# Kernel tuning notes

Hardware: AMD Instinct MI355X
Metric: run time of the kernel (lower is better)

## Reference

```python
import jax, jax.numpy as jnp
import numpy as np


def setup_inputs() -> dict:
    key = jax.random.key(0)
    ks = jax.random.split(key, 9)
    B, S, F = 16, 512, 1024
    scale = 1.0 / np.sqrt(2 * F)  # ~torch Linear init scale
    return {
        "v": jax.random.normal(ks[0], (B, S, F), jnp.float32),
        "t": jax.random.normal(ks[1], (B, S, F), jnp.float32),
        "a": jax.random.normal(ks[2], (B, S, F), jnp.float32),
        "W_tv": jax.random.normal(ks[3], (2 * F, F), jnp.float32) * scale,
        "b_tv": jnp.zeros((F,), jnp.float32),
        "W_ta": jax.random.normal(ks[4], (2 * F, F), jnp.float32) * scale,
        "b_ta": jnp.zeros((F,), jnp.float32),
        "W_av": jax.random.normal(ks[5], (2 * F, F), jnp.float32) * scale,
        "b_av": jnp.zeros((F,), jnp.float32),
    }


def _branch_feat(x1, x2, W, b):
    # tanh(Linear(cat(x1, x2)))  -- split weight to avoid materializing concat
    F = x1.shape[-1]
    W1, W2 = W[:F], W[F:]
    return jnp.tanh(jnp.einsum("bsf,fg->bsg", x1, W1)
                    + jnp.einsum("bsf,fg->bsg", x2, W2) + b)


def _attend_gate(q, feat):
    # softmax(q @ feat^T) @ q, gated by feat
    scores = jnp.einsum("bqf,bkf->bqk", q, feat)  # [B,S,S]
    p = jax.nn.softmax(scores, axis=-1)
    return jnp.einsum("bqk,bkf->bqf", p, q) * feat


def reference(v, t, a, W_tv, b_tv, W_ta, b_ta, W_av, b_av):
    Ftv = _branch_feat(t, v, W_tv, b_tv)
    Fta = _branch_feat(t, a, W_ta, b_ta)
    Fav = _branch_feat(a, v, W_av, b_av)
    Oatv = _attend_gate(a, Ftv)
    Ovta = _attend_gate(v, Fta)
    Otav = _attend_gate(t, Fav)
    return jnp.concatenate((Oatv, Ovta, Otav), axis=2)
```

## Files before the change

kernel.cpp:

```cpp
#include <hip/hip_runtime.h>

typedef unsigned short ushort_t;
typedef _Float16 f16x8 __attribute__((ext_vector_type(8)));
typedef float f32x4 __attribute__((ext_vector_type(4)));
typedef unsigned short u16x8 __attribute__((ext_vector_type(8)));

#define DEVINL __device__ __forceinline__

constexpr int B = 16, S = 512, F = 1024;
constexpr int M_ROWS = B * S;
constexpr size_t NX = (size_t)M_ROWS * F;
constexpr size_t NW = (size_t)F * (2 * F);
constexpr size_t NSC = (size_t)3 * B * S * S;

DEVINL ushort_t f2h(float f) { return __builtin_bit_cast(ushort_t, (_Float16)f); }
DEVINL float h2f(ushort_t h) { return (float)__builtin_bit_cast(_Float16, h); }

DEVINL void gload_lds16(const void* g, void* l) {
  __builtin_amdgcn_global_load_lds(
      (__attribute__((address_space(1))) void*)(g),
      (__attribute__((address_space(3))) void*)(l), 16, 0, 0);
}

DEVINL f32x4 mfma16h(f16x8 a, f16x8 b, f32x4 c) {
  return __builtin_amdgcn_mfma_f32_16x16x32_f16(a, b, c, 0, 0, 0);
}

template <int KSTEPS, int SPLIT_STEP>
DEVINL void gemm4p_core(const ushort_t* __restrict__ a1, const ushort_t* __restrict__ a2,
                        int lda, const ushort_t* __restrict__ bsrc, int ldb,
                        ushort_t* lds, int tid, f32x4 (&acc)[4][8]) {
  constexpr int BUF = 32768;
  constexpr int BOFF = 16384;
  constexpr int KM = KSTEPS - 1;
  const int lane = tid & 63, w = tid >> 6;
  const int wr = (w >> 1) * 64, wc = (w & 1) * 128;
  const int slog = (lane & 7) ^ ((lane >> 3) & 7);

  const int sl0 = ((lane >> 4) ^ (lane & 7)) * 8;
  const int sl1 = ((4 + (lane >> 4)) ^ (lane & 7)) * 8;
  const ushort_t* dsA0 = lds + (wr + (lane & 15)) * 64 + sl0;
  const ushort_t* dsA1 = lds + (wr + (lane & 15)) * 64 + sl1;
  const ushort_t* dsB0 = lds + BOFF + (wc + (lane & 15)) * 64 + sl0;
  const ushort_t* dsB1 = lds + BOFF + (wc + (lane & 15)) * 64 + sl1;

  const size_t ldaS = (size_t)lda, ldbS = (size_t)ldb;
  const ushort_t* gA1 = a1 + (size_t)(w * 16 + (lane >> 3)) * ldaS + slog * 8;
  const ushort_t* gA2 = a2 + (size_t)(w * 16 + (lane >> 3)) * ldaS + slog * 8;
  const ushort_t* gB  = bsrc + (size_t)(w * 16 + (lane >> 3)) * ldbS + slog * 8;
  ushort_t* dA = lds + (w * 16) * 64;
  ushort_t* dB = lds + BOFF + (w * 16) * 64;

  auto stA = [&](int bb, int ks, int h) {
    const ushort_t* base = ((SPLIT_STEP >= KSTEPS) || (ks < SPLIT_STEP)) ? gA1 : gA2;
    const ushort_t* s = base + (ks & (SPLIT_STEP - 1)) * 64 + (size_t)(h * 128) * ldaS;
    ushort_t* d = dA + bb * BUF + h * 8192;
    gload_lds16(s, d);
    gload_lds16(s + 8 * ldaS, d + 512);
  };
  auto stB = [&](int bb, int ks, int h) {
    const ushort_t* s = gB + ks * 64 + (size_t)(h * 128) * ldbS;
    ushort_t* d = dB + bb * BUF + h * 8192;
    gload_lds16(s, d);
    gload_lds16(s + 8 * ldbS, d + 512);
  };

#define BAR asm volatile("s_barrier" ::: "memory")
#define RDB(J)                                              \
  Bn0 = *(const f16x8*)(rB0 + (J) * 1024);                  \
  Bn1 = *(const f16x8*)(rB1 + (J) * 1024);                  \
  Bn2 = *(const f16x8*)(rB0 + ((J) + 1) * 1024);            \
  Bn3 = *(const f16x8*)(rB1 + ((J) + 1) * 1024);
#define PHASE_MM(JP)                                        \
  __builtin_amdgcn_s_setprio(1);                            \
  _Pragma("unroll")                                         \
  for (int i = 0; i < 4; ++i) {                             \
    acc[i][2 * (JP)]     = mfma16h(rA[i][0], Bc0, acc[i][2 * (JP)]);     \
    acc[i][2 * (JP)]     = mfma16h(rA[i][1], Bc1, acc[i][2 * (JP)]);     \
    acc[i][2 * (JP) + 1] = mfma16h(rA[i][0], Bc2, acc[i][2 * (JP) + 1]); \
    acc[i][2 * (JP) + 1] = mfma16h(rA[i][1], Bc3, acc[i][2 * (JP) + 1]); \
  }                                                         \
  __builtin_amdgcn_s_setprio(0);
#define SWAPB  Bc0 = Bn0; Bc1 = Bn1; Bc2 = Bn2; Bc3 = Bn3;
#define TILE(BB, T) {                                       \
  const int ksB = ((T) + 1) & KM;                           \
  const int ksA = ((T) + 2) & KM;                           \
  const ushort_t* rA0 = dsA0 + (BB) * BUF;                  \
  const ushort_t* rA1 = dsA1 + (BB) * BUF;                  \
  const ushort_t* rB0 = dsB0 + (BB) * BUF;                  \
  const ushort_t* rB1 = dsB1 + (BB) * BUF;                  \
  f16x8 rA[4][2];                                           \
  f16x8 Bc0, Bc1, Bc2, Bc3, Bn0, Bn1, Bn2, Bn3;             \
  _Pragma("unroll")                                         \
  for (int i = 0; i < 4; ++i) {                             \
    rA[i][0] = *(const f16x8*)(rA0 + i * 1024);             \
    rA[i][1] = *(const f16x8*)(rA1 + i * 1024);             \
  }                                                         \
  Bc0 = *(const f16x8*)(rB0);                               \
  Bc1 = *(const f16x8*)(rB1);                               \
  Bc2 = *(const f16x8*)(rB0 + 1024);                        \
  Bc3 = *(const f16x8*)(rB1 + 1024);                        \
  RDB(2)                                                    \
  stB(BB ^ 1, ksB, 0);                                      \
  BAR; PHASE_MM(0) BAR;                                     \
  SWAPB RDB(4)                                              \
  stB(BB ^ 1, ksB, 1);                                      \
  BAR; PHASE_MM(1) BAR;                                     \
  SWAPB RDB(6)                                              \
  stA(BB, ksA, 0);                                          \
  BAR; PHASE_MM(2) BAR;                                     \
  SWAPB                                                     \
  stA(BB, ksA, 1);                                          \
  BAR; PHASE_MM(3)                                          \
  asm volatile("s_waitcnt vmcnt(4)" ::: "memory");          \
  BAR;                                                      \
}

  stA(0, 0, 0); stA(0, 0, 1);
  stB(0, 0, 0); stB(0, 0, 1);
  stA(1, 1 & KM, 0); stA(1, 1 & KM, 1);
  asm volatile("s_waitcnt vmcnt(4)" ::: "memory");
  BAR;

  for (int t = 0; t < KSTEPS; t += 2) {
    TILE(0, t)
    TILE(1, t + 1)
  }
#undef TILE
#undef SWAPB
#undef PHASE_MM
#undef RDB
#undef BAR
}

__global__ __launch_bounds__(256) void split_x_kernel(
    const float* __restrict__ v, const float* __restrict__ t, const float* __restrict__ a,
    ushort_t* __restrict__ xh, ushort_t* __restrict__ xT) {
  __shared__ ushort_t tile[64][65];
  int mod = blockIdx.z;
  const float* src = (mod == 0) ? v : (mod == 1 ? t : a);
  int b = blockIdx.y;
  int s0 = (blockIdx.x >> 4) * 64;
  int f0 = (blockIdx.x & 15) * 64;
  int tid = threadIdx.x;
  ushort_t* xp = xh + mod * NX;
  ushort_t* xt = xT + mod * NX;
  int fl = (tid & 15) * 4;
#pragma unroll
  for (int r = 0; r < 4; ++r) {
    int sl = (tid >> 4) + r * 16;
    int row = b * S + s0 + sl;
    float4 x = *(const float4*)(src + (size_t)row * F + f0 + fl);
    ushort_t h0 = f2h(x.x), h1 = f2h(x.y), h2 = f2h(x.z), h3 = f2h(x.w);
    *(ushort4*)(xp + (size_t)row * F + f0 + fl) = make_ushort4(h0, h1, h2, h3);
    tile[sl][fl] = h0; tile[sl][fl + 1] = h1; tile[sl][fl + 2] = h2; tile[sl][fl + 3] = h3;
  }
  __syncthreads();
#pragma unroll
  for (int r = 0; r < 4; ++r) {
    int flr = (tid >> 4) + r * 16;
    int sl4 = (tid & 15) * 4;
    ushort4 o = make_ushort4(tile[sl4][flr], tile[sl4 + 1][flr],
                             tile[sl4 + 2][flr], tile[sl4 + 3][flr]);
    size_t tidx = ((size_t)(b * F + f0 + flr)) * S + s0 + sl4;
    *(ushort4*)(xt + tidx) = o;
  }
}

__global__ __launch_bounds__(256) void split_w_kernel(
    const float* __restrict__ w0, const float* __restrict__ w1, const float* __restrict__ w2,
    ushort_t* __restrict__ wtpack) {
  __shared__ ushort_t th[64][65];
  int br = blockIdx.z;
  const float* w = (br == 0) ? w0 : (br == 1 ? w1 : w2);
  int g0 = blockIdx.x * 64;
  int f0 = blockIdx.y * 64;
  int tid = threadIdx.x;
  int gl = (tid & 15) * 4;
#pragma unroll
  for (int r = 0; r < 4; ++r) {
    int fl = (tid >> 4) + r * 16;
    float4 x = *(const float4*)(w + (size_t)(f0 + fl) * F + g0 + gl);
    th[fl][gl] = f2h(x.x); th[fl][gl + 1] = f2h(x.y);
    th[fl][gl + 2] = f2h(x.z); th[fl][gl + 3] = f2h(x.w);
  }
  __syncthreads();
  ushort_t* op = wtpack + br * NW;
#pragma unroll
  for (int r = 0; r < 4; ++r) {
    int glr = (tid >> 4) + r * 16;
    int fl4 = (tid & 15) * 4;
    size_t o = (size_t)(g0 + glr) * (2 * F) + f0 + fl4;
    *(ushort4*)(op + o) = make_ushort4(th[fl4][glr], th[fl4 + 1][glr],
                                       th[fl4 + 2][glr], th[fl4 + 3][glr]);
  }
}

__global__ __launch_bounds__(512, 2) void feat_gemm_kernel(
    const ushort_t* __restrict__ xh, const ushort_t* __restrict__ wtpack,
    const float* __restrict__ b0, const float* __restrict__ b1, const float* __restrict__ b2,
    ushort_t* __restrict__ fpack) {
  constexpr int M1[3] = {1, 1, 2};
  constexpr int M2[3] = {0, 2, 0};
  __shared__ __attribute__((aligned(16))) ushort_t lds[2 * 32768];
  int br = blockIdx.z;
  int lin = blockIdx.x;
  int gm0 = ((lin & 7) * 4 + ((lin >> 3) & 3)) * 256;
  int gn0 = (lin >> 5) * 256;
  int tid = threadIdx.x, lane = tid & 63, w = tid >> 6;
  const ushort_t* a1 = xh + M1[br] * NX + (size_t)gm0 * F;
  const ushort_t* a2 = xh + M2[br] * NX + (size_t)gm0 * F;
  const ushort_t* bb = wtpack + br * NW + (size_t)gn0 * (2 * F);
  f32x4 acc[4][8] = {};
  gemm4p_core<32, 16>(a1, a2, F, bb, 2 * F, lds, tid, acc);
  const float* bias = (br == 0) ? b0 : (br == 1 ? b1 : b2);
  ushort_t* op = fpack + br * NX;
  int wr = (w >> 1) * 64, wc = (w & 1) * 128;
#pragma unroll
  for (int i = 0; i < 4; ++i)
#pragma unroll
    for (int j = 0; j < 8; ++j)
#pragma unroll
      for (int r = 0; r < 4; ++r) {
        int row = gm0 + wr + i * 16 + (lane >> 4) * 4 + r;
        int col = gn0 + wc + j * 16 + (lane & 15);
        op[(size_t)row * F + col] = f2h(tanhf(acc[i][j][r] + bias[col]));
      }
}

__global__ __launch_bounds__(512, 2) void scores_gemm_kernel(
    const ushort_t* __restrict__ xh, const ushort_t* __restrict__ fpack,
    float* __restrict__ scores) {
  constexpr int QM[3] = {2, 0, 1};
  __shared__ __attribute__((aligned(16))) ushort_t lds[2 * 32768];
  int z = blockIdx.z;
  int br = z >> 4, b = z & 15;
  int gm0 = blockIdx.x * 256;
  int gn0 = blockIdx.y * 256;
  int tid = threadIdx.x, lane = tid & 63, w = tid >> 6;
  const ushort_t* a1 = xh + QM[br] * NX + (size_t)(b * S + gm0) * F;
  const ushort_t* bb = fpack + br * NX + (size_t)(b * S + gn0) * F;
  f32x4 acc[4][8] = {};
  gemm4p_core<16, 16>(a1, a1, F, bb, F, lds, tid, acc);
  float* out = scores + (size_t)z * S * S;
  int wr = (w >> 1) * 64, wc = (w & 1) * 128;
#pragma unroll
  for (int i = 0; i < 4; ++i)
#pragma unroll
    for (int j = 0; j < 8; ++j)
#pragma unroll
      for (int r = 0; r < 4; ++r) {
        int row = gm0 + wr + i * 16 + (lane >> 4) * 4 + r;
        int col = gn0 + wc + j * 16 + (lane & 15);
        out[(size_t)row * S + col] = acc[i][j][r];
      }
}

__global__ __launch_bounds__(256) void softmax_kernel(
    const float* __restrict__ scores, ushort_t* __restrict__ p) {
  int wave = threadIdx.x >> 6, lane = threadIdx.x & 63;
  int row = blockIdx.x * 4 + wave;
  const float* src = scores + (size_t)row * S;
  float4 v0 = *(const float4*)(src + lane * 8);
  float4 v1 = *(const float4*)(src + lane * 8 + 4);
  float m = fmaxf(fmaxf(fmaxf(v0.x, v0.y), fmaxf(v0.z, v0.w)),
                  fmaxf(fmaxf(v1.x, v1.y), fmaxf(v1.z, v1.w)));
#pragma unroll
  for (int d = 1; d < 64; d <<= 1) m = fmaxf(m, __shfl_xor(m, d));
  float e[8] = {expf(v0.x - m), expf(v0.y - m), expf(v0.z - m), expf(v0.w - m),
                expf(v1.x - m), expf(v1.y - m), expf(v1.z - m), expf(v1.w - m)};
  float s = ((e[0] + e[1]) + (e[2] + e[3])) + ((e[4] + e[5]) + (e[6] + e[7]));
#pragma unroll
  for (int d = 1; d < 64; d <<= 1) s += __shfl_xor(s, d);
  float inv = 1.0f / s;
  u16x8 o;
#pragma unroll
  for (int j = 0; j < 8; ++j) o[j] = f2h(e[j] * inv);
  *(u16x8*)(p + (size_t)row * S + lane * 8) = o;
}

__global__ __launch_bounds__(512, 2) void pv_gemm_kernel(
    const ushort_t* __restrict__ p, const ushort_t* __restrict__ xT,
    const ushort_t* __restrict__ fpack, float* __restrict__ out) {
  constexpr int QM[3] = {2, 0, 1};
  __shared__ __attribute__((aligned(16))) ushort_t lds[2 * 32768];
  int z = blockIdx.z;
  int br = z >> 4, b = z & 15;
  int gm0 = blockIdx.x * 256;
  int gn0 = blockIdx.y * 256;
  int tid = threadIdx.x, lane = tid & 63, w = tid >> 6;
  const ushort_t* pa = p + (size_t)z * S * S + (size_t)gm0 * S;
  const ushort_t* qt = xT + QM[br] * NX + (size_t)b * F * S + (size_t)gn0 * S;
  f32x4 acc[4][8] = {};
  gemm4p_core<8, 8>(pa, pa, S, qt, S, lds, tid, acc);
  const ushort_t* fp = fpack + br * NX;
  int wr = (w >> 1) * 64, wc = (w & 1) * 128;
#pragma unroll
  for (int i = 0; i < 4; ++i)
#pragma unroll
    for (int j = 0; j < 8; ++j)
#pragma unroll
      for (int r = 0; r < 4; ++r) {
        int row = gm0 + wr + i * 16 + (lane >> 4) * 4 + r;
        int col = gn0 + wc + j * 16 + (lane & 15);
        float fe = h2f(fp[(size_t)(b * S + row) * F + col]);
        out[(size_t)(b * S + row) * (3 * F) + br * F + col] = acc[i][j][r] * fe;
      }
}

extern "C" void kernel_launch(void* const* d_in, const int* in_sizes, int n_in,
                              void* d_out, int out_size, void* d_ws, size_t ws_size,
                              hipStream_t stream) {
  (void)in_sizes; (void)n_in; (void)out_size; (void)ws_size;
  const float* v = (const float*)d_in[0];
  const float* t = (const float*)d_in[1];
  const float* a = (const float*)d_in[2];
  const float* W_tv = (const float*)d_in[3];
  const float* b_tv = (const float*)d_in[4];
  const float* W_ta = (const float*)d_in[5];
  const float* b_ta = (const float*)d_in[6];
  const float* W_av = (const float*)d_in[7];
  const float* b_av = (const float*)d_in[8];
  float* out = (float*)d_out;

  ushort_t* xh = (ushort_t*)d_ws;
  ushort_t* xT = xh + 3 * NX;
  ushort_t* wtpack = xT + 3 * NX;
  ushort_t* fpack = wtpack + 3 * NW;
  float* scores = (float*)(fpack + 3 * NX);
  ushort_t* pbuf = (ushort_t*)(scores + NSC);

  split_x_kernel<<<dim3(128, 16, 3), 256, 0, stream>>>(v, t, a, xh, xT);
  split_w_kernel<<<dim3(16, 32, 3), 256, 0, stream>>>(W_tv, W_ta, W_av, wtpack);
  feat_gemm_kernel<<<dim3(128, 1, 3), 512, 0, stream>>>(xh, wtpack,
                                                        b_tv, b_ta, b_av, fpack);
  scores_gemm_kernel<<<dim3(2, 2, 48), 512, 0, stream>>>(xh, fpack, scores);
  softmax_kernel<<<dim3((3 * B * S) / 4), 256, 0, stream>>>(scores, pbuf);
  pv_gemm_kernel<<<dim3(2, 4, 48), 512, 0, stream>>>(pbuf, xT, fpack, out);
}
```

Before: 295.2 us.

## Fuse softmax into scores GEMM with full-row tiles and triple-buffered loads

Replaces the separate scores GEMM and softmax kernels with one kernel. Each block computes a 128x512 tile, covering a full row of keys, and does max, exp and normalisation in registers with a cross-wave reduction through LDS. This removes the fp32 scores round trip through global memory and one kernel launch. It also uses a triple-buffered direct-to-LDS load pipeline with a new tile shape. The cost is fewer blocks (192 instead of 192x... same count, but smaller M tiles) and a larger LDS footprint that may limit occupancy.

```diff
diff --git a/kernel.cpp b/kernel.cpp
--- a/kernel.cpp
+++ b/kernel.cpp
@@ -11,7 +11,6 @@
 constexpr int M_ROWS = B * S;
 constexpr size_t NX = (size_t)M_ROWS * F;
 constexpr size_t NW = (size_t)F * (2 * F);
-constexpr size_t NSC = (size_t)3 * B * S * S;
 
 DEVINL ushort_t f2h(float f) { return __builtin_bit_cast(ushort_t, (_Float16)f); }
 DEVINL float h2f(ushort_t h) { return (float)__builtin_bit_cast(_Float16, h); }
@@ -228,55 +227,127 @@
       }
 }
 
-__global__ __launch_bounds__(512, 2) void scores_gemm_kernel(
+__global__ __launch_bounds__(512, 2) void attn_scores_kernel(
     const ushort_t* __restrict__ xh, const ushort_t* __restrict__ fpack,
-    float* __restrict__ scores) {
+    ushort_t* __restrict__ pbuf) {
   constexpr int QM[3] = {2, 0, 1};
-  __shared__ __attribute__((aligned(16))) ushort_t lds[2 * 32768];
+  constexpr int BUFE = 20480;
+  constexpr int BOFFE = 4096;
+  __shared__ __attribute__((aligned(16))) ushort_t lds[3 * BUFE + 1024];
+  float* redm = (float*)(lds + 3 * BUFE);
   int z = blockIdx.z;
   int br = z >> 4, b = z & 15;
-  int gm0 = blockIdx.x * 256;
-  int gn0 = blockIdx.y * 256;
+  int gm0 = blockIdx.x * 128;
   int tid = threadIdx.x, lane = tid & 63, w = tid >> 6;
-  const ushort_t* a1 = xh + QM[br] * NX + (size_t)(b * S + gm0) * F;
-  const ushort_t* bb = fpack + br * NX + (size_t)(b * S + gn0) * F;
+  int wm = w >> 2, wn = w & 3;
+  int wr = wm * 64, wc = wn * 128;
+  const ushort_t* qa = xh + QM[br] * NX + (size_t)(b * S + gm0) * F;
+  const ushort_t* kb = fpack + br * NX + (size_t)(b * S) * F;
+
+  const int scol = (((lane & 3) ^ ((lane >> 3) & 3)) * 8);
+  const int foff = (lane & 15) * 32 + (((lane >> 4) ^ ((lane >> 1) & 3)) * 8);
+
+  auto stA = [&](int sb, int ks) {
+    const ushort_t* s = qa + (size_t)(w * 16 + (lane >> 2)) * F + ks * 32 + scol;
+    gload_lds16(s, lds + sb * BUFE + w * 512);
+  };
+  auto stB = [&](int sb, int ks) {
+#pragma unroll
+    for (int g = 0; g < 4; ++g) {
+      const ushort_t* s = kb + (size_t)(w * 64 + g * 16 + (lane >> 2)) * F + ks * 32 + scol;
+      gload_lds16(s, lds + sb * BUFE + BOFFE + w * 2048 + g * 512);
+    }
+  };
+
   f32x4 acc[4][8] = {};
-  gemm4p_core<16, 16>(a1, a1, F, bb, F, lds, tid, acc);
-  float* out = scores + (size_t)z * S * S;
-  int wr = (w >> 1) * 64, wc = (w & 1) * 128;
+  stA(0, 0); stB(0, 0);
+  stA(1, 1); stB(1, 1);
+  asm volatile("s_waitcnt vmcnt(5)" ::: "memory");
+  asm volatile("s_barrier" ::: "memory");
+
+  for (int t = 0; t < 32; ++t) {
+    const int cb = t % 3, sb = (t + 2) % 3;
+    const int ks = (t + 2) & 31;
+    stA(sb, ks); stB(sb, ks);
+    const ushort_t* L = lds + cb * BUFE;
+    f16x8 rA[4], rB[8];
+#pragma unroll
+    for (int i = 0; i < 4; ++i) rA[i] = *(const f16x8*)(L + (wr + i * 16) * 32 + foff);
+#pragma unroll
+    for (int j = 0; j < 8; ++j)
+      rB[j] = *(const f16x8*)(L + BOFFE + (wc + j * 16) * 32 + foff);
+    __builtin_amdgcn_s_setprio(1);
+#pragma unroll
+    for (int j = 0; j < 8; ++j)
+#pragma unroll
+      for (int i = 0; i < 4; ++i) acc[i][j] = mfma16h(rA[i], rB[j], acc[i][j]);
+    __builtin_amdgcn_s_setprio(0);
+    asm volatile("s_waitcnt vmcnt(5)" ::: "memory");
+    asm volatile("s_barrier" ::: "memory");
+  }
+
+  float mx[4][4];
 #pragma unroll
   for (int i = 0; i < 4; ++i)
 #pragma unroll
-    for (int j = 0; j < 8; ++j)
-#pragma unroll
-      for (int r = 0; r < 4; ++r) {
-        int row = gm0 + wr + i * 16 + (lane >> 4) * 4 + r;
-        int col = gn0 + wc + j * 16 + (lane & 15);
-        out[(size_t)row * S + col] = acc[i][j][r];
+    for (int r = 0; r < 4; ++r) {
+      float m = acc[i][0][r];
+#pragma unroll
+      for (int j = 1; j < 8; ++j) m = fmaxf(m, acc[i][j][r]);
+#pragma unroll
+      for (int d = 1; d < 16; d <<= 1) m = fmaxf(m, __shfl_xor(m, d));
+      mx[i][r] = m;
+    }
+  if ((lane & 15) == 0) {
+#pragma unroll
+    for (int i = 0; i < 4; ++i)
+#pragma unroll
+      for (int r = 0; r < 4; ++r)
+        redm[wn * 128 + wr + i * 16 + (lane >> 4) * 4 + r] = mx[i][r];
+  }
+  __syncthreads();
+  float inv[4][4];
+#pragma unroll
+  for (int i = 0; i < 4; ++i)
+#pragma unroll
+    for (int r = 0; r < 4; ++r) {
+      int row = wr + i * 16 + (lane >> 4) * 4 + r;
+      float fm = fmaxf(fmaxf(redm[row], redm[128 + row]),
+                       fmaxf(redm[256 + row], redm[384 + row]));
+      float s = 0.f;
+#pragma unroll
+      for (int j = 0; j < 8; ++j) {
+        float e = expf(acc[i][j][r] - fm);
+        acc[i][j][r] = e;
+        s += e;
       }
-}
-
-__global__ __launch_bounds__(256) void softmax_kernel(
-    const float* __restrict__ scores, ushort_t* __restrict__ p) {
-  int wave = threadIdx.x >> 6, lane = threadIdx.x & 63;
-  int row = blockIdx.x * 4 + wave;
-  const float* src = scores + (size_t)row * S;
-  float4 v0 = *(const float4*)(src + lane * 8);
-  float4 v1 = *(const float4*)(src + lane * 8 + 4);
-  float m = fmaxf(fmaxf(fmaxf(v0.x, v0.y), fmaxf(v0.z, v0.w)),
-                  fmaxf(fmaxf(v1.x, v1.y), fmaxf(v1.z, v1.w)));
-#pragma unroll
-  for (int d = 1; d < 64; d <<= 1) m = fmaxf(m, __shfl_xor(m, d));
-  float e[8] = {expf(v0.x - m), expf(v0.y - m), expf(v0.z - m), expf(v0.w - m),
-                expf(v1.x - m), expf(v1.y - m), expf(v1.z - m), expf(v1.w - m)};
-  float s = ((e[0] + e[1]) + (e[2] + e[3])) + ((e[4] + e[5]) + (e[6] + e[7]));
-#pragma unroll
-  for (int d = 1; d < 64; d <<= 1) s += __shfl_xor(s, d);
-  float inv = 1.0f / s;
-  u16x8 o;
-#pragma unroll
-  for (int j = 0; j < 8; ++j) o[j] = f2h(e[j] * inv);
-  *(u16x8*)(p + (size_t)row * S + lane * 8) = o;
+#pragma unroll
+      for (int d = 1; d < 16; d <<= 1) s += __shfl_xor(s, d);
+      inv[i][r] = s;
+    }
+  __syncthreads();
+  if ((lane & 15) == 0) {
+#pragma unroll
+    for (int i = 0; i < 4; ++i)
+#pragma unroll
+      for (int r = 0; r < 4; ++r)
+        redm[wn * 128 + wr + i * 16 + (lane >> 4) * 4 + r] = inv[i][r];
+  }
+  __syncthreads();
+  ushort_t* pout = pbuf + (size_t)z * S * S;
+#pragma unroll
+  for (int i = 0; i < 4; ++i)
+#pragma unroll
+    for (int r = 0; r < 4; ++r) {
+      int row = wr + i * 16 + (lane >> 4) * 4 + r;
+      float fs = (redm[row] + redm[128 + row]) + (redm[256 + row] + redm[384 + row]);
+      float fi = 1.0f / fs;
+#pragma unroll
+      for (int j = 0; j < 8; ++j) {
+        int col = wc + j * 16 + (lane & 15);
+        pout[(size_t)(gm0 + row) * S + col] = f2h(acc[i][j][r] * fi);
+      }
+    }
 }
 
 __global__ __launch_bounds__(512, 2) void pv_gemm_kernel(
@@ -327,14 +398,12 @@
   ushort_t* xT = xh + 3 * NX;
   ushort_t* wtpack = xT + 3 * NX;
   ushort_t* fpack = wtpack + 3 * NW;
-  float* scores = (float*)(fpack + 3 * NX);
-  ushort_t* pbuf = (ushort_t*)(scores + NSC);
+  ushort_t* pbuf = fpack + 3 * NX;
 
   split_x_kernel<<<dim3(128, 16, 3), 256, 0, stream>>>(v, t, a, xh, xT);
   split_w_kernel<<<dim3(16, 32, 3), 256, 0, stream>>>(W_tv, W_ta, W_av, wtpack);
   feat_gemm_kernel<<<dim3(128, 1, 3), 512, 0, stream>>>(xh, wtpack,
                                                         b_tv, b_ta, b_av, fpack);
-  scores_gemm_kernel<<<dim3(2, 2, 48), 512, 0, stream>>>(xh, fpack, scores);
-  softmax_kernel<<<dim3((3 * B * S) / 4), 256, 0, stream>>>(scores, pbuf);
+  attn_scores_kernel<<<dim3(4, 1, 48), 512, 0, stream>>>(xh, fpack, pbuf);
   pv_gemm_kernel<<<dim3(2, 4, 48), 512, 0, stream>>>(pbuf, xT, fpack, out);
 }
```

Result: no change. 290.2 us (median of 2 runs) (-1.7%).
